# Kernel optimization log

Hardware: AMD Instinct MI355X
Metric: run time of the kernel (lower is better)

The kernel has to match this reference:

```python
import jax, jax.numpy as jnp
import numpy as np

B, S, D, H = 4, 2048, 1024, 16
DH = D // H  # attention_head_size = 64


def setup_inputs() -> dict:
    key = jax.random.key(0)
    ks = jax.random.split(key, 9)
    scale = 1.0 / np.sqrt(D)
    x = jax.random.normal(ks[0], (B, S, D), dtype=jnp.float32)
    Wq = jax.random.normal(ks[1], (H, D, DH), dtype=jnp.float32) * scale
    Wk = jax.random.normal(ks[2], (H, D, DH), dtype=jnp.float32) * scale
    Wv = jax.random.normal(ks[3], (H, D, DH), dtype=jnp.float32) * scale
    bq = jax.random.normal(ks[4], (H, DH), dtype=jnp.float32) * 0.01
    bk = jax.random.normal(ks[5], (H, DH), dtype=jnp.float32) * 0.01
    bv = jax.random.normal(ks[6], (H, DH), dtype=jnp.float32) * 0.01
    Wo = jax.random.normal(ks[7], (D, D), dtype=jnp.float32) * scale
    bo = jax.random.normal(ks[8], (D,), dtype=jnp.float32) * 0.01
    return {"x": x, "Wq": Wq, "bq": bq, "Wk": Wk, "bk": bk,
            "Wv": Wv, "bv": bv, "Wo": Wo, "bo": bo}


def reference(x, Wq, bq, Wk, bk, Wv, bv, Wo, bo):
    # Per-head Linear projections, stacked over the head axis h.
    q = jnp.einsum('bsd,hde->bhse', x, Wq) + bq[None, :, None, :]
    k = jnp.einsum('bsd,hde->bhse', x, Wk) + bk[None, :, None, :]
    v = jnp.einsum('bsd,hde->bhse', x, Wv) + bv[None, :, None, :]
    # QK^T / sqrt(dh), softmax over keys (axis=-1), then @ V.
    scores = jnp.einsum('bhse,bhte->bhst', q, k) / jnp.sqrt(jnp.float32(DH))
    attn = jax.nn.softmax(scores, axis=-1)
    ctx = jnp.einsum('bhst,bhte->bhse', attn, v)
    # Concatenate heads along the feature axis: [B,S,H*DH].
    concat = jnp.transpose(ctx, (0, 2, 1, 3)).reshape(B, S, H * DH)
    # Output projection (dropout is identity in inference).
    return concat @ Wo + bo
```

## Files before the change

kernel.cpp:

```cpp
#include <hip/hip_runtime.h>


#define Bn  4
#define Sn  2048
#define Dn  1024
#define Hn  16
#define DHn 64
#define Mn  (Bn*Sn)
#define LDKV 72

typedef unsigned short u16;
typedef __attribute__((ext_vector_type(8))) short short8;
typedef __attribute__((ext_vector_type(4))) short short4v;
typedef __attribute__((ext_vector_type(4))) float f32x4;
typedef __attribute__((ext_vector_type(2))) unsigned int uint2v;

__device__ __forceinline__ u16 f2bf(float f) {
  unsigned u = __float_as_uint(f);
  return (u16)((u + 0x7FFFu + ((u >> 16) & 1u)) >> 16);
}

__device__ __forceinline__ void async16(const void* g, void* l) {
  __builtin_amdgcn_global_load_lds(
      (const __attribute__((address_space(1))) void*)g,
      (__attribute__((address_space(3))) void*)l, 16, 0, 0);
}

__device__ __forceinline__ unsigned pk2(float a, float b) {
  return __builtin_amdgcn_perm(__float_as_uint(b), __float_as_uint(a), 0x07060302u);
}

__global__ __launch_bounds__(256) void k_convert_x(
    const float4* __restrict__ x, ushort4* __restrict__ xb, int n4) {
  int i = blockIdx.x * 256 + threadIdx.x;
  if (i < n4) {
    float4 f = x[i];
    ushort4 o;
    o.x = f2bf(f.x); o.y = f2bf(f.y); o.z = f2bf(f.z); o.w = f2bf(f.w);
    xb[i] = o;
  }
}

__global__ __launch_bounds__(256) void k_convert_w(
    const float* __restrict__ Wq, const float* __restrict__ Wk,
    const float* __restrict__ Wv, const float* __restrict__ Wo,
    u16* __restrict__ WqT, u16* __restrict__ WkT,
    u16* __restrict__ WvT, u16* __restrict__ WoT) {
  __shared__ float t[64][65];
  const int bid = blockIdx.x;
  const int wsel = bid >> 8;
  const int idx = bid & 255;
  const int tid = threadIdx.x;
  const int c = tid & 63;
  const int r4 = tid >> 6;

  if (wsel < 3) {
    const float* W = (wsel == 0) ? Wq : (wsel == 1) ? Wk : Wv;
    u16* T = (wsel == 0) ? WqT : (wsel == 1) ? WkT : WvT;
    const int h = idx >> 4;
    const int d0 = (idx & 15) * 64;
    const float* src = W + (size_t)h * (Dn * DHn) + (size_t)d0 * DHn;
#pragma unroll
    for (int r = 0; r < 16; r++) {
      int row = r * 4 + r4;
      t[row][c] = src[row * DHn + c];
    }
    __syncthreads();
    u16* dst = T + (size_t)(h * 64) * Dn + d0;
#pragma unroll
    for (int r = 0; r < 16; r++) {
      int erow = r * 4 + r4;
      dst[(size_t)erow * Dn + c] = f2bf(t[c][erow]);
    }
  } else {
    const int n0 = (idx >> 4) * 64;
    const int d0 = (idx & 15) * 64;
#pragma unroll
    for (int r = 0; r < 16; r++) {
      int row = r * 4 + r4;
      t[row][c] = Wo[(size_t)(d0 + row) * Dn + n0 + c];
    }
    __syncthreads();
#pragma unroll
    for (int r = 0; r < 16; r++) {
      int nrow = r * 4 + r4;
      WoT[(size_t)(n0 + nrow) * Dn + d0 + c] = f2bf(t[c][nrow]);
    }
  }
}

template<int SWAP>
__global__ __launch_bounds__(512) void k_gemm_qkv(
    const u16* __restrict__ A, const u16* __restrict__ B0T,
    const u16* __restrict__ B1T, const float* __restrict__ bias0,
    const float* __restrict__ bias1, u16* __restrict__ out0,
    u16* __restrict__ out1) {
  const int z = blockIdx.z;
  const u16* BT = z ? B1T : B0T;
  const float* bias = z ? bias1 : bias0;
  u16* dst = z ? out1 : out0;
  const int tile_m = blockIdx.x * 128;
  const int tile_n = blockIdx.y * 128;
  const int K = Dn;

  __shared__ u16 As[128 * 64];
  __shared__ u16 Bs[128 * 64];

  const int tid = threadIdx.x;
  const int lane = tid & 63;
  const int wave = tid >> 6;
  const int wm = wave & 3, wn = wave >> 2;
  const int quad = lane >> 4, l16 = lane & 15;
  const int srow8 = lane >> 3;
  const int gchunk = (lane & 7) ^ srow8;
  const int sw = l16 & 7;

  f32x4 acc[2][4];
#pragma unroll
  for (int i = 0; i < 2; i++)
#pragma unroll
    for (int j = 0; j < 4; j++) acc[i][j] = (f32x4){0.f, 0.f, 0.f, 0.f};

  for (int k0 = 0; k0 < K; k0 += 64) {
    const int rb = wave * 16;
    async16(&A[(size_t)(tile_m + rb + srow8) * K + k0 + gchunk * 8], &As[rb * 64]);
    async16(&A[(size_t)(tile_m + rb + 8 + srow8) * K + k0 + gchunk * 8], &As[(rb + 8) * 64]);
    async16(&BT[(size_t)(tile_n + rb + srow8) * K + k0 + gchunk * 8], &Bs[rb * 64]);
    async16(&BT[(size_t)(tile_n + rb + 8 + srow8) * K + k0 + gchunk * 8], &Bs[(rb + 8) * 64]);
    __syncthreads();
#pragma unroll
    for (int ks = 0; ks < 2; ++ks) {
      short8 a[2], b[4];
#pragma unroll
      for (int i = 0; i < 2; i++)
        a[i] = *(const short8*)&As[(wm * 32 + i * 16 + l16) * 64 + ((ks * 4 + quad) ^ sw) * 8];
#pragma unroll
      for (int j = 0; j < 4; j++)
        b[j] = *(const short8*)&Bs[(wn * 64 + j * 16 + l16) * 64 + ((ks * 4 + quad) ^ sw) * 8];
#pragma unroll
      for (int i = 0; i < 2; i++)
#pragma unroll
        for (int j = 0; j < 4; j++)
          acc[i][j] = SWAP
              ? __builtin_amdgcn_mfma_f32_16x16x32_bf16(b[j], a[i], acc[i][j], 0, 0, 0)
              : __builtin_amdgcn_mfma_f32_16x16x32_bf16(a[i], b[j], acc[i][j], 0, 0, 0);
    }
    __syncthreads();
  }

  if (SWAP) {
    const float scale = (z == 0) ? 0.18033688011112042f : 1.0f;
#pragma unroll
    for (int i = 0; i < 2; i++) {
      const int s = tile_m + wm * 32 + i * 16 + l16;
      const int bb = s >> 11, sl = s & 2047;
#pragma unroll
      for (int j = 0; j < 4; j++) {
        const int nb = tile_n + wn * 64 + j * 16 + quad * 4;
        const float4 b4 = *(const float4*)&bias[nb];
        const int h = nb >> 6, e0 = nb & 63;
        ushort4 o;
        o.x = f2bf((acc[i][j][0] + b4.x) * scale);
        o.y = f2bf((acc[i][j][1] + b4.y) * scale);
        o.z = f2bf((acc[i][j][2] + b4.z) * scale);
        o.w = f2bf((acc[i][j][3] + b4.w) * scale);
        *(ushort4*)&dst[((size_t)(bb * Hn + h) * Sn + sl) * DHn + e0] = o;
      }
    }
  } else {
#pragma unroll
    for (int i = 0; i < 2; i++) {
      const int s0 = tile_m + wm * 32 + i * 16 + quad * 4;
      const int bb = s0 >> 11, sl = s0 & 2047;
#pragma unroll
      for (int j = 0; j < 4; j++) {
        const int n = tile_n + wn * 64 + j * 16 + l16;
        const int h = n >> 6, e = n & 63;
        const float bn = bias[n];
        ushort4 o;
        o.x = f2bf(acc[i][j][0] + bn);
        o.y = f2bf(acc[i][j][1] + bn);
        o.z = f2bf(acc[i][j][2] + bn);
        o.w = f2bf(acc[i][j][3] + bn);
        *(ushort4*)&dst[((size_t)(bb * Hn + h) * DHn + e) * Sn + sl] = o;
      }
    }
  }
}

__global__ __launch_bounds__(256) void k_attn(
    const u16* __restrict__ qg, const u16* __restrict__ kg,
    const u16* __restrict__ vg, u16* __restrict__ ctx) {
  const int bh = blockIdx.y;
  const int b = bh >> 4, h = bh & 15;
  const int tid = threadIdx.x;
  const int wave = tid >> 6, lane = tid & 63;
  const int quad = lane >> 4, l16 = lane & 15;
  const int qbase = blockIdx.x * 128 + wave * 32;

  const u16* qp = qg + (size_t)bh * Sn * DHn;
  const u16* kp = kg + (size_t)bh * Sn * DHn;
  const u16* vp = vg + (size_t)bh * DHn * Sn;

  __shared__ u16 Ks[2][64 * 64];
  __shared__ u16 Vs[2][64 * LDKV];

  const int srow8 = lane >> 3;
  const int gchunk = (lane & 7) ^ srow8;
  const int sw = l16 & 7;

  const int vrow = tid >> 3;
  const int vc = tid & 7;

  short8 bq[2][2];
#pragma unroll
  for (int g2 = 0; g2 < 2; g2++) {
    bq[g2][0] = *(const short8*)&qp[(size_t)(qbase + g2 * 16 + l16) * DHn + quad * 8];
    bq[g2][1] = *(const short8*)&qp[(size_t)(qbase + g2 * 16 + l16) * DHn + 32 + quad * 8];
  }

  f32x4 octx[2][4];
#pragma unroll
  for (int g2 = 0; g2 < 2; g2++)
#pragma unroll
    for (int j = 0; j < 4; j++) octx[g2][j] = (f32x4){0.f, 0.f, 0.f, 0.f};
  float lr[2] = {0.f, 0.f};

  {
    const int rbase = wave * 16;
    async16(&kp[(size_t)(rbase + srow8) * DHn + gchunk * 8], &Ks[0][rbase * 64]);
    async16(&kp[(size_t)(rbase + 8 + srow8) * DHn + gchunk * 8], &Ks[0][(rbase + 8) * 64]);
    uint4 vv0 = *(const uint4*)&vp[(size_t)vrow * Sn + vc * 8];
    uint4 vv1 = *(const uint4*)&vp[(size_t)(32 + vrow) * Sn + vc * 8];
    *(uint4*)&Vs[0][vrow * LDKV + vc * 8] = vv0;
    *(uint4*)&Vs[0][(32 + vrow) * LDKV + vc * 8] = vv1;
  }
  __syncthreads();

  uint4 vv0, vv1;
  for (int kt = 0; kt < Sn / 64; ++kt) {
    const int cur = kt & 1, nxt = cur ^ 1;
    const bool more = (kt + 1 < Sn / 64);
    if (more) {
      const int key1 = (kt + 1) * 64;
      const int rbase = wave * 16;
      async16(&kp[(size_t)(key1 + rbase + srow8) * DHn + gchunk * 8], &Ks[nxt][rbase * 64]);
      async16(&kp[(size_t)(key1 + rbase + 8 + srow8) * DHn + gchunk * 8], &Ks[nxt][(rbase + 8) * 64]);
      vv0 = *(const uint4*)&vp[(size_t)vrow * Sn + key1 + vc * 8];
      vv1 = *(const uint4*)&vp[(size_t)(32 + vrow) * Sn + key1 + vc * 8];
    }

    short4v ap[2][4];
#pragma unroll
    for (int g = 0; g < 4; g++) {
      short8 ka0 = *(const short8*)&Ks[cur][(g * 16 + l16) * 64 + (quad ^ sw) * 8];
      short8 ka1 = *(const short8*)&Ks[cur][(g * 16 + l16) * 64 + ((quad + 4) ^ sw) * 8];
#pragma unroll
      for (int g2 = 0; g2 < 2; g2++) {
        f32x4 sc = (f32x4){0.f, 0.f, 0.f, 0.f};
        sc = __builtin_amdgcn_mfma_f32_16x16x32_bf16(ka0, bq[g2][0], sc, 0, 0, 0);
        sc = __builtin_amdgcn_mfma_f32_16x16x32_bf16(ka1, bq[g2][1], sc, 0, 0, 0);
        float p[4];
#pragma unroll
        for (int r = 0; r < 4; r++) p[r] = __builtin_amdgcn_exp2f(sc[r]);
        lr[g2] += (p[0] + p[1]) + (p[2] + p[3]);
        ap[g2][g] = __builtin_bit_cast(short4v,
            (uint2v){pk2(p[0], p[1]), pk2(p[2], p[3])});
      }
    }

#pragma unroll
    for (int j = 0; j < 4; j++) {
#pragma unroll
      for (int g = 0; g < 4; g++) {
        short4v vb = *(const short4v*)&Vs[cur][(j * 16 + l16) * LDKV + g * 16 + quad * 4];
        octx[0][j] = __builtin_amdgcn_mfma_f32_16x16x16bf16_1k(ap[0][g], vb, octx[0][j], 0, 0, 0);
        octx[1][j] = __builtin_amdgcn_mfma_f32_16x16x16bf16_1k(ap[1][g], vb, octx[1][j], 0, 0, 0);
      }
    }

    if (more) {
      *(uint4*)&Vs[nxt][vrow * LDKV + vc * 8] = vv0;
      *(uint4*)&Vs[nxt][(32 + vrow) * LDKV + vc * 8] = vv1;
    }
    __syncthreads();
  }

#pragma unroll
  for (int g2 = 0; g2 < 2; g2++) {
    lr[g2] += __shfl_xor(lr[g2], 16, 64);
    lr[g2] += __shfl_xor(lr[g2], 32, 64);
  }
  float rl[2][4];
#pragma unroll
  for (int g2 = 0; g2 < 2; g2++)
#pragma unroll
    for (int r = 0; r < 4; r++)
      rl[g2][r] = 1.0f / __shfl(lr[g2], quad * 4 + r, 64);

#pragma unroll
  for (int g2 = 0; g2 < 2; g2++)
#pragma unroll
    for (int j = 0; j < 4; j++) {
      const int n = h * DHn + j * 16 + l16;
#pragma unroll
      for (int r = 0; r < 4; r++) {
        const int s = qbase + g2 * 16 + quad * 4 + r;
        ctx[(size_t)(b * Sn + s) * Dn + n] = f2bf(octx[g2][j][r] * rl[g2][r]);
      }
    }
}

__global__ __launch_bounds__(512) void k_gemm_out(
    const u16* __restrict__ A, const u16* __restrict__ WoT,
    const float* __restrict__ bo, float* __restrict__ out) {
  const int tile_m = blockIdx.x * 128;
  const int tile_n = blockIdx.y * 128;
  const int K = Dn;

  __shared__ u16 As[128 * 64];
  __shared__ u16 Bs[128 * 64];

  const int tid = threadIdx.x;
  const int lane = tid & 63;
  const int wave = tid >> 6;
  const int wm = wave & 3, wn = wave >> 2;
  const int quad = lane >> 4, l16 = lane & 15;
  const int srow8 = lane >> 3;
  const int gchunk = (lane & 7) ^ srow8;
  const int sw = l16 & 7;

  f32x4 acc[2][4];
#pragma unroll
  for (int i = 0; i < 2; i++)
#pragma unroll
    for (int j = 0; j < 4; j++) acc[i][j] = (f32x4){0.f, 0.f, 0.f, 0.f};

  for (int k0 = 0; k0 < K; k0 += 64) {
    const int rb = wave * 16;
    async16(&A[(size_t)(tile_m + rb + srow8) * K + k0 + gchunk * 8], &As[rb * 64]);
    async16(&A[(size_t)(tile_m + rb + 8 + srow8) * K + k0 + gchunk * 8], &As[(rb + 8) * 64]);
    async16(&WoT[(size_t)(tile_n + rb + srow8) * K + k0 + gchunk * 8], &Bs[rb * 64]);
    async16(&WoT[(size_t)(tile_n + rb + 8 + srow8) * K + k0 + gchunk * 8], &Bs[(rb + 8) * 64]);
    __syncthreads();
#pragma unroll
    for (int ks = 0; ks < 2; ++ks) {
      short8 a[2], b[4];
#pragma unroll
      for (int i = 0; i < 2; i++)
        a[i] = *(const short8*)&As[(wm * 32 + i * 16 + l16) * 64 + ((ks * 4 + quad) ^ sw) * 8];
#pragma unroll
      for (int j = 0; j < 4; j++)
        b[j] = *(const short8*)&Bs[(wn * 64 + j * 16 + l16) * 64 + ((ks * 4 + quad) ^ sw) * 8];
#pragma unroll
      for (int i = 0; i < 2; i++)
#pragma unroll
        for (int j = 0; j < 4; j++)
          acc[i][j] = __builtin_amdgcn_mfma_f32_16x16x32_bf16(b[j], a[i], acc[i][j], 0, 0, 0);
    }
    __syncthreads();
  }

#pragma unroll
  for (int i = 0; i < 2; i++) {
    const int s = tile_m + wm * 32 + i * 16 + l16;
#pragma unroll
    for (int j = 0; j < 4; j++) {
      const int nb = tile_n + wn * 64 + j * 16 + quad * 4;
      const float4 b4 = *(const float4*)&bo[nb];
      float4 o;
      o.x = acc[i][j][0] + b4.x;
      o.y = acc[i][j][1] + b4.y;
      o.z = acc[i][j][2] + b4.z;
      o.w = acc[i][j][3] + b4.w;
      *(float4*)&out[(size_t)s * Dn + nb] = o;
    }
  }
}

extern "C" void kernel_launch(void* const* d_in, const int* in_sizes, int n_in,
                              void* d_out, int out_size, void* d_ws, size_t ws_size,
                              hipStream_t stream) {
  const float* x  = (const float*)d_in[0];
  const float* Wq = (const float*)d_in[1];
  const float* bq = (const float*)d_in[2];
  const float* Wk = (const float*)d_in[3];
  const float* bk = (const float*)d_in[4];
  const float* Wv = (const float*)d_in[5];
  const float* bv = (const float*)d_in[6];
  const float* Wo = (const float*)d_in[7];
  const float* bo = (const float*)d_in[8];
  float* out = (float*)d_out;

  char* ws = (char*)d_ws;
  u16* xb  = (u16*)ws;  ws += (size_t)Mn * Dn * 2;
  u16* WqT = (u16*)ws;  ws += (size_t)Dn * Dn * 2;
  u16* WkT = (u16*)ws;  ws += (size_t)Dn * Dn * 2;
  u16* WvT = (u16*)ws;  ws += (size_t)Dn * Dn * 2;
  u16* WoT = (u16*)ws;  ws += (size_t)Dn * Dn * 2;
  u16* qb  = (u16*)ws;  ws += (size_t)Mn * Dn * 2;
  u16* kb  = (u16*)ws;  ws += (size_t)Mn * Dn * 2;
  u16* vtb = (u16*)ws;  ws += (size_t)Mn * Dn * 2;
  u16* ctx = xb;

  k_convert_x<<<(Mn * Dn / 4) / 256, 256, 0, stream>>>((const float4*)x, (ushort4*)xb, Mn * Dn / 4);
  k_convert_w<<<1024, 256, 0, stream>>>(Wq, Wk, Wv, Wo, WqT, WkT, WvT, WoT);

  dim3 g1(Mn / 128, Dn / 128, 2);
  k_gemm_qkv<1><<<g1, 512, 0, stream>>>(xb, WqT, WkT, bq, bk, qb, kb);
  dim3 g1v(Mn / 128, Dn / 128, 1);
  k_gemm_qkv<0><<<g1v, 512, 0, stream>>>(xb, WvT, nullptr, bv, nullptr, vtb, nullptr);

  dim3 g2(Sn / 128, Bn * Hn);
  k_attn<<<g2, 256, 0, stream>>>(qb, kb, vtb, ctx);

  dim3 g3(Mn / 128, Dn / 128);
  k_gemm_out<<<g3, 512, 0, stream>>>(ctx, WoT, bo, out);
}
```

Measured before the change: 285.9 us.

## Merge QKV GEMM launches, async swizzled V loads, MFMA row-sums, XCD-aware attention grid

Folds the Q/K and V projection GEMMs into one launch with a z=3 grid, and writes V transposed from the swapped MFMA layout using strided scalar stores. In attention, V tiles now go through async global-to-LDS copies with the same XOR swizzle as K, replacing register staging and the padded layout. Softmax denominators come from an extra MFMA against a ones vector instead of scalar adds and cross-lane shuffles. The kernel also raises wave priority around the PV MFMAs and remaps the block index so blocks sharing a head land on the same XCD for L2 reuse. The V epilogue's scattered 2-byte stores may cost more write bandwidth.

```diff
diff --git a/kernel.cpp b/kernel.cpp
--- a/kernel.cpp
+++ b/kernel.cpp
@@ -7,7 +7,6 @@
 #define Hn  16
 #define DHn 64
 #define Mn  (Bn*Sn)
-#define LDKV 72
 
 typedef unsigned short u16;
 typedef __attribute__((ext_vector_type(8))) short short8;
@@ -89,16 +88,15 @@
   }
 }
 
-template<int SWAP>
 __global__ __launch_bounds__(512) void k_gemm_qkv(
-    const u16* __restrict__ A, const u16* __restrict__ B0T,
-    const u16* __restrict__ B1T, const float* __restrict__ bias0,
-    const float* __restrict__ bias1, u16* __restrict__ out0,
-    u16* __restrict__ out1) {
+    const u16* __restrict__ A, const u16* __restrict__ WqT,
+    const u16* __restrict__ WkT, const u16* __restrict__ WvT,
+    const float* __restrict__ bqv, const float* __restrict__ bkv,
+    const float* __restrict__ bvv, u16* __restrict__ qb,
+    u16* __restrict__ kb, u16* __restrict__ vtb) {
   const int z = blockIdx.z;
-  const u16* BT = z ? B1T : B0T;
-  const float* bias = z ? bias1 : bias0;
-  u16* dst = z ? out1 : out0;
+  const u16* BT = (z == 0) ? WqT : (z == 1) ? WkT : WvT;
+  const float* bias = (z == 0) ? bqv : (z == 1) ? bkv : bvv;
   const int tile_m = blockIdx.x * 128;
   const int tile_n = blockIdx.y * 128;
   const int K = Dn;
@@ -141,15 +139,14 @@
       for (int i = 0; i < 2; i++)
 #pragma unroll
         for (int j = 0; j < 4; j++)
-          acc[i][j] = SWAP
-              ? __builtin_amdgcn_mfma_f32_16x16x32_bf16(b[j], a[i], acc[i][j], 0, 0, 0)
-              : __builtin_amdgcn_mfma_f32_16x16x32_bf16(a[i], b[j], acc[i][j], 0, 0, 0);
-    }
-    __syncthreads();
-  }
-
-  if (SWAP) {
-    const float scale = (z == 0) ? 0.18033688011112042f : 1.0f;
+          acc[i][j] = __builtin_amdgcn_mfma_f32_16x16x32_bf16(b[j], a[i], acc[i][j], 0, 0, 0);
+    }
+    __syncthreads();
+  }
+
+  const float scale = (z == 0) ? 0.18033688011112042f : 1.0f;
+  if (z < 2) {
+    u16* dst = z ? kb : qb;
 #pragma unroll
     for (int i = 0; i < 2; i++) {
       const int s = tile_m + wm * 32 + i * 16 + l16;
@@ -170,19 +167,18 @@
   } else {
 #pragma unroll
     for (int i = 0; i < 2; i++) {
-      const int s0 = tile_m + wm * 32 + i * 16 + quad * 4;
-      const int bb = s0 >> 11, sl = s0 & 2047;
+      const int s = tile_m + wm * 32 + i * 16 + l16;
+      const int bb = s >> 11, sl = s & 2047;
 #pragma unroll
       for (int j = 0; j < 4; j++) {
-        const int n = tile_n + wn * 64 + j * 16 + l16;
-        const int h = n >> 6, e = n & 63;
-        const float bn = bias[n];
-        ushort4 o;
-        o.x = f2bf(acc[i][j][0] + bn);
-        o.y = f2bf(acc[i][j][1] + bn);
-        o.z = f2bf(acc[i][j][2] + bn);
-        o.w = f2bf(acc[i][j][3] + bn);
-        *(ushort4*)&dst[((size_t)(bb * Hn + h) * DHn + e) * Sn + sl] = o;
+        const int nb = tile_n + wn * 64 + j * 16 + quad * 4;
+        const float4 b4 = *(const float4*)&bias[nb];
+        const int h = nb >> 6, e0 = nb & 63;
+        u16* vd = &vtb[((size_t)(bb * Hn + h) * DHn + e0) * Sn + sl];
+        vd[0]            = f2bf(acc[i][j][0] + b4.x);
+        vd[(size_t)Sn]   = f2bf(acc[i][j][1] + b4.y);
+        vd[(size_t)2*Sn] = f2bf(acc[i][j][2] + b4.z);
+        vd[(size_t)3*Sn] = f2bf(acc[i][j][3] + b4.w);
       }
     }
   }
@@ -191,26 +187,26 @@
 __global__ __launch_bounds__(256) void k_attn(
     const u16* __restrict__ qg, const u16* __restrict__ kg,
     const u16* __restrict__ vg, u16* __restrict__ ctx) {
-  const int bh = blockIdx.y;
+  const int p = blockIdx.x;
+  const int logical = (p & 7) * 128 + (p >> 3);
+  const int bh = logical >> 4;
   const int b = bh >> 4, h = bh & 15;
   const int tid = threadIdx.x;
   const int wave = tid >> 6, lane = tid & 63;
   const int quad = lane >> 4, l16 = lane & 15;
-  const int qbase = blockIdx.x * 128 + wave * 32;
+  const int qbase = (logical & 15) * 128 + wave * 32;
 
   const u16* qp = qg + (size_t)bh * Sn * DHn;
   const u16* kp = kg + (size_t)bh * Sn * DHn;
   const u16* vp = vg + (size_t)bh * DHn * Sn;
 
   __shared__ u16 Ks[2][64 * 64];
-  __shared__ u16 Vs[2][64 * LDKV];
+  __shared__ u16 Vs[2][64 * 64];
 
   const int srow8 = lane >> 3;
   const int gchunk = (lane & 7) ^ srow8;
   const int sw = l16 & 7;
-
-  const int vrow = tid >> 3;
-  const int vc = tid & 7;
+  const int rbase = wave * 16;
 
   short8 bq[2][2];
 #pragma unroll
@@ -224,30 +220,25 @@
   for (int g2 = 0; g2 < 2; g2++)
 #pragma unroll
     for (int j = 0; j < 4; j++) octx[g2][j] = (f32x4){0.f, 0.f, 0.f, 0.f};
-  float lr[2] = {0.f, 0.f};
-
-  {
-    const int rbase = wave * 16;
-    async16(&kp[(size_t)(rbase + srow8) * DHn + gchunk * 8], &Ks[0][rbase * 64]);
-    async16(&kp[(size_t)(rbase + 8 + srow8) * DHn + gchunk * 8], &Ks[0][(rbase + 8) * 64]);
-    uint4 vv0 = *(const uint4*)&vp[(size_t)vrow * Sn + vc * 8];
-    uint4 vv1 = *(const uint4*)&vp[(size_t)(32 + vrow) * Sn + vc * 8];
-    *(uint4*)&Vs[0][vrow * LDKV + vc * 8] = vv0;
-    *(uint4*)&Vs[0][(32 + vrow) * LDKV + vc * 8] = vv1;
-  }
+  f32x4 octl[2];
+  octl[0] = (f32x4){0.f, 0.f, 0.f, 0.f};
+  octl[1] = (f32x4){0.f, 0.f, 0.f, 0.f};
+  const short4v vones = {(short)0x3F80, (short)0x3F80, (short)0x3F80, (short)0x3F80};
+
+  async16(&kp[(size_t)(rbase + srow8) * DHn + gchunk * 8], &Ks[0][rbase * 64]);
+  async16(&kp[(size_t)(rbase + 8 + srow8) * DHn + gchunk * 8], &Ks[0][(rbase + 8) * 64]);
+  async16(&vp[(size_t)(rbase + srow8) * Sn + gchunk * 8], &Vs[0][rbase * 64]);
+  async16(&vp[(size_t)(rbase + 8 + srow8) * Sn + gchunk * 8], &Vs[0][(rbase + 8) * 64]);
   __syncthreads();
 
-  uint4 vv0, vv1;
   for (int kt = 0; kt < Sn / 64; ++kt) {
     const int cur = kt & 1, nxt = cur ^ 1;
-    const bool more = (kt + 1 < Sn / 64);
-    if (more) {
+    if (kt + 1 < Sn / 64) {
       const int key1 = (kt + 1) * 64;
-      const int rbase = wave * 16;
       async16(&kp[(size_t)(key1 + rbase + srow8) * DHn + gchunk * 8], &Ks[nxt][rbase * 64]);
       async16(&kp[(size_t)(key1 + rbase + 8 + srow8) * DHn + gchunk * 8], &Ks[nxt][(rbase + 8) * 64]);
-      vv0 = *(const uint4*)&vp[(size_t)vrow * Sn + key1 + vc * 8];
-      vv1 = *(const uint4*)&vp[(size_t)(32 + vrow) * Sn + key1 + vc * 8];
+      async16(&vp[(size_t)(rbase + srow8) * Sn + key1 + gchunk * 8], &Vs[nxt][rbase * 64]);
+      async16(&vp[(size_t)(rbase + 8 + srow8) * Sn + key1 + gchunk * 8], &Vs[nxt][(rbase + 8) * 64]);
     }
 
     short4v ap[2][4];
@@ -260,43 +251,39 @@
         f32x4 sc = (f32x4){0.f, 0.f, 0.f, 0.f};
         sc = __builtin_amdgcn_mfma_f32_16x16x32_bf16(ka0, bq[g2][0], sc, 0, 0, 0);
         sc = __builtin_amdgcn_mfma_f32_16x16x32_bf16(ka1, bq[g2][1], sc, 0, 0, 0);
-        float p[4];
-#pragma unroll
-        for (int r = 0; r < 4; r++) p[r] = __builtin_amdgcn_exp2f(sc[r]);
-        lr[g2] += (p[0] + p[1]) + (p[2] + p[3]);
-        ap[g2][g] = __builtin_bit_cast(short4v,
-            (uint2v){pk2(p[0], p[1]), pk2(p[2], p[3])});
+        float pp[4];
+#pragma unroll
+        for (int r = 0; r < 4; r++) pp[r] = __builtin_amdgcn_exp2f(sc[r]);
+        ap[g2][g] = __builtin_bit_cast(short4v, (uint2v){pk2(pp[0], pp[1]), pk2(pp[2], pp[3])});
       }
     }
 
+    __builtin_amdgcn_s_setprio(1);
+#pragma unroll
+    for (int g = 0; g < 4; g++) {
+      octl[0] = __builtin_amdgcn_mfma_f32_16x16x16bf16_1k(ap[0][g], vones, octl[0], 0, 0, 0);
+      octl[1] = __builtin_amdgcn_mfma_f32_16x16x16bf16_1k(ap[1][g], vones, octl[1], 0, 0, 0);
+    }
 #pragma unroll
     for (int j = 0; j < 4; j++) {
 #pragma unroll
       for (int g = 0; g < 4; g++) {
-        short4v vb = *(const short4v*)&Vs[cur][(j * 16 + l16) * LDKV + g * 16 + quad * 4];
+        short4v vb = *(const short4v*)&Vs[cur][(j * 16 + l16) * 64 +
+            ((g * 2 + (quad >> 1)) ^ sw) * 8 + (quad & 1) * 4];
         octx[0][j] = __builtin_amdgcn_mfma_f32_16x16x16bf16_1k(ap[0][g], vb, octx[0][j], 0, 0, 0);
         octx[1][j] = __builtin_amdgcn_mfma_f32_16x16x16bf16_1k(ap[1][g], vb, octx[1][j], 0, 0, 0);
       }
     }
-
-    if (more) {
-      *(uint4*)&Vs[nxt][vrow * LDKV + vc * 8] = vv0;
-      *(uint4*)&Vs[nxt][(32 + vrow) * LDKV + vc * 8] = vv1;
-    }
-    __syncthreads();
-  }
-
-#pragma unroll
-  for (int g2 = 0; g2 < 2; g2++) {
-    lr[g2] += __shfl_xor(lr[g2], 16, 64);
-    lr[g2] += __shfl_xor(lr[g2], 32, 64);
-  }
+    __builtin_amdgcn_s_setprio(0);
+    __syncthreads();
+  }
+
   float rl[2][4];
 #pragma unroll
   for (int g2 = 0; g2 < 2; g2++)
 #pragma unroll
     for (int r = 0; r < 4; r++)
-      rl[g2][r] = 1.0f / __shfl(lr[g2], quad * 4 + r, 64);
+      rl[g2][r] = 1.0f / octl[g2][r];
 
 #pragma unroll
   for (int g2 = 0; g2 < 2; g2++)
@@ -406,13 +393,10 @@
   k_convert_x<<<(Mn * Dn / 4) / 256, 256, 0, stream>>>((const float4*)x, (ushort4*)xb, Mn * Dn / 4);
   k_convert_w<<<1024, 256, 0, stream>>>(Wq, Wk, Wv, Wo, WqT, WkT, WvT, WoT);
 
-  dim3 g1(Mn / 128, Dn / 128, 2);
-  k_gemm_qkv<1><<<g1, 512, 0, stream>>>(xb, WqT, WkT, bq, bk, qb, kb);
-  dim3 g1v(Mn / 128, Dn / 128, 1);
-  k_gemm_qkv<0><<<g1v, 512, 0, stream>>>(xb, WvT, nullptr, bv, nullptr, vtb, nullptr);
-
-  dim3 g2(Sn / 128, Bn * Hn);
-  k_attn<<<g2, 256, 0, stream>>>(qb, kb, vtb, ctx);
+  dim3 g1(Mn / 128, Dn / 128, 3);
+  k_gemm_qkv<<<g1, 512, 0, stream>>>(xb, WqT, WkT, WvT, bq, bk, bv, qb, kb, vtb);
+
+  k_attn<<<(Sn / 128) * Bn * Hn, 256, 0, stream>>>(qb, kb, vtb, ctx);
 
   dim3 g3(Mn / 128, Dn / 128);
   k_gemm_out<<<g3, 512, 0, stream>>>(ctx, WoT, bo, out);
```

Result: slower. 304.8 us (+6.6%).
